# Kernel optimization log

Hardware: AMD Instinct MI355X
Metric: run time of the kernel (lower is better)

## Reference

```python
import jax, jax.numpy as jnp
import numpy as np


def setup_inputs() -> dict:
    key = jax.random.key(0)
    k_tok, k_lp = jax.random.split(key)
    R, S, V = 512, 1024, 50257  # rows = bsz*beam, seq_len, vocab
    tokens = jax.random.randint(k_tok, (R, S), 0, V, dtype=jnp.int64)
    lprobs = jax.random.normal(k_lp, (R, V), dtype=jnp.float32)
    return {
        "tokens": tokens,
        "lprobs": lprobs,
        "bsz": 128,
        "step": 1020,
        "beam_size": 4,
        "no_repeat_ngram_size": 3,
    }


def reference(tokens, lprobs, bsz, step, beam_size, no_repeat_ngram_size):
    # Semantics of fairseq's ngram_repeat_block CUDA kernel:
    # for each row, if tokens[row, i:i+n-1] == tokens[row, step-n+2:step+1]
    # for any window start i in [0, step-n+1], ban token tokens[row, i+n-1].
    n = no_repeat_ngram_size
    R = tokens.shape[0]
    V = lprobs.shape[1]
    num_windows = step - n + 2  # static Python int

    last = tokens[:, step - n + 2 : step + 1]            # (R, n-1) final (n-1)-gram
    starts = jnp.arange(num_windows)
    win_idx = starts[:, None] + jnp.arange(n - 1)[None, :]  # (W, n-1)
    prefixes = tokens[:, win_idx]                        # (R, W, n-1)
    match = jnp.all(prefixes == last[:, None, :], axis=-1)  # (R, W) bool
    banned = tokens[:, starts + (n - 1)]                 # (R, W) tokens to ban

    # Scatter -inf into matched banned positions; unmatched windows point
    # out-of-range (index V) and are dropped.
    scatter_idx = jnp.where(match, banned, V)            # (R, W)
    rows = jnp.arange(R)[:, None]
    return lprobs.at[rows, scatter_idx].set(-jnp.inf, mode="drop")
```

## Files before the change

kernel.cpp:

```cpp
#include <hip/hip_runtime.h>
#include <math.h>

__global__ void __launch_bounds__(256)
ngram_copy(const float4* __restrict__ in4, float4* __restrict__ out4,
           const float* __restrict__ in, float* __restrict__ out,
           int n4, int tail) {
    int i = blockIdx.x * 256 + threadIdx.x;
    if (i < n4) out4[i] = in4[i];
    if (blockIdx.x == 0 && threadIdx.x < tail) {
        int t = n4 * 4 + threadIdx.x;
        out[t] = in[t];
    }
}

__global__ void __launch_bounds__(256)
ngram_ban(const int* __restrict__ tokens, float* __restrict__ out,
          const int* __restrict__ bsz_p, const int* __restrict__ step_p,
          const int* __restrict__ beam_p, const int* __restrict__ n_p,
          long long tok_elems, long long lp_elems) {
    const int bsz  = *bsz_p;
    const int step = *step_p;
    const int beam = *beam_p;
    const int n    = *n_p;

    const int R = bsz * beam;
    const long long S = tok_elems / R;
    const long long V = lp_elems / R;
    const int num_windows = step - n + 2;
    const int last_start  = step - n + 2;
    const int L = n - 1;

    for (int r = blockIdx.x; r < R; r += gridDim.x) {
        const int* __restrict__ trow = tokens + (long long)r * S;
        for (int j = threadIdx.x; j < num_windows; j += blockDim.x) {
            bool m = true;
            for (int k = 0; k < L; ++k) {
                m &= (trow[j + k] == trow[last_start + k]);
            }
            if (m) {
                const int banned = trow[j + n - 1];
                out[(long long)r * V + banned] = -INFINITY;
            }
        }
    }
}

extern "C" void kernel_launch(void* const* d_in, const int* in_sizes, int n_in,
                              void* d_out, int out_size, void* d_ws, size_t ws_size,
                              hipStream_t stream) {
    const int*   tokens = (const int*)d_in[0];
    const float* lprobs = (const float*)d_in[1];
    const int*   bsz_p  = (const int*)d_in[2];
    const int*   step_p = (const int*)d_in[3];
    const int*   beam_p = (const int*)d_in[4];
    const int*   n_p    = (const int*)d_in[5];
    float* out = (float*)d_out;

    {
        const int n4   = out_size / 4;
        const int tail = out_size - n4 * 4;
        const int blocks = (n4 + 255) / 256;
        ngram_copy<<<blocks, 256, 0, stream>>>(
            (const float4*)lprobs, (float4*)out, lprobs, out, n4, tail);
    }

    {
        const int blocks = 512;
        ngram_ban<<<blocks, 256, 0, stream>>>(
            tokens, out, bsz_p, step_p, beam_p, n_p,
            (long long)in_sizes[0], (long long)in_sizes[1]);
    }
}
```

Before: 191.5 us.

## Use hipMemcpyAsync for lprobs copy and cache last n-gram in registers

Replaces the custom float4 copy kernel with a device-to-device hipMemcpyAsync, relying on the runtime's copy path (possibly a DMA/SDMA engine or a tuned blit kernel). In the ban kernel, the final (n-1)-gram is loaded once per row into a small register array instead of being reread from global memory for every window. The register array is fixed at 7 entries, so n-gram sizes above 8 would compare incorrectly, and the memcpy's speed depends on which copy path the runtime picks.

New measurement: 195.3 us. Within noise of the previous version (+1.9%).

```diff
diff --git a/kernel.cpp b/kernel.cpp
--- a/kernel.cpp
+++ b/kernel.cpp
@@ -1,17 +1,6 @@
 #include <hip/hip_runtime.h>
 #include <math.h>
 
-__global__ void __launch_bounds__(256)
-ngram_copy(const float4* __restrict__ in4, float4* __restrict__ out4,
-           const float* __restrict__ in, float* __restrict__ out,
-           int n4, int tail) {
-    int i = blockIdx.x * 256 + threadIdx.x;
-    if (i < n4) out4[i] = in4[i];
-    if (blockIdx.x == 0 && threadIdx.x < tail) {
-        int t = n4 * 4 + threadIdx.x;
-        out[t] = in[t];
-    }
-}
 
 __global__ void __launch_bounds__(256)
 ngram_ban(const int* __restrict__ tokens, float* __restrict__ out,
@@ -32,10 +21,16 @@
 
     for (int r = blockIdx.x; r < R; r += gridDim.x) {
         const int* __restrict__ trow = tokens + (long long)r * S;
+
+        int last[7];
+        #pragma unroll
+        for (int k = 0; k < 7; ++k)
+            last[k] = (k < L) ? trow[last_start + k] : 0;
+
         for (int j = threadIdx.x; j < num_windows; j += blockDim.x) {
             bool m = true;
             for (int k = 0; k < L; ++k) {
-                m &= (trow[j + k] == trow[last_start + k]);
+                m &= (trow[j + k] == last[k]);
             }
             if (m) {
                 const int banned = trow[j + n - 1];
@@ -56,18 +51,10 @@
     const int*   n_p    = (const int*)d_in[5];
     float* out = (float*)d_out;
 
-    {
-        const int n4   = out_size / 4;
-        const int tail = out_size - n4 * 4;
-        const int blocks = (n4 + 255) / 256;
-        ngram_copy<<<blocks, 256, 0, stream>>>(
-            (const float4*)lprobs, (float4*)out, lprobs, out, n4, tail);
-    }
+    hipMemcpyAsync(out, lprobs, (size_t)out_size * sizeof(float),
+                   hipMemcpyDeviceToDevice, stream);
 
-    {
-        const int blocks = 512;
-        ngram_ban<<<blocks, 256, 0, stream>>>(
-            tokens, out, bsz_p, step_p, beam_p, n_p,
-            (long long)in_sizes[0], (long long)in_sizes[1]);
-    }
+    ngram_ban<<<512, 256, 0, stream>>>(
+        tokens, out, bsz_p, step_p, beam_p, n_p,
+        (long long)in_sizes[0], (long long)in_sizes[1]);
 }
```
